# Kernel tuning notes

Hardware: AMD Instinct MI355X
Metric: run time of the kernel (lower is better)

## Reference

```python
import jax, jax.numpy as jnp
import numpy as np

B, C, N, M = 8, 128, 2048, 512

def setup_inputs() -> dict:
    key = jax.random.key(0)
    k1, k2, k3, k4 = jax.random.split(key, 4)
    scale = 1.0 / np.sqrt(C)
    x = jax.random.normal(k1, (B, C, N), dtype=jnp.float32)
    # conv1d with kernel size 1 and no bias == channel-mixing matmul, weight [C_out, C_in]
    Wq = jax.random.normal(k2, (C, C), dtype=jnp.float32) * scale
    Wk = jax.random.normal(k3, (C, C), dtype=jnp.float32) * scale
    Wv = jax.random.normal(k4, (C, C), dtype=jnp.float32) * scale
    return {"x": x, "Wq": Wq, "Wk": Wk, "Wv": Wv, "npts_ds": M}

def reference(x, Wq, Wk, Wv, npts_ds):
    # q,k,v: [B,C,N] via 1x1 conv == einsum over input channels
    q = jnp.einsum('oc,bcn->bon', Wq, x)
    k = jnp.einsum('oc,bcn->bon', Wk, x)
    v = jnp.einsum('oc,bcn->bon', Wv, x)
    # energy: [B,N,N] = q^T k (contract channel dim)
    energy = jnp.einsum('bcn,bcm->bnm', q, k)
    scale_factor = jnp.sqrt(jnp.asarray(q.shape[-2], dtype=energy.dtype))  # sqrt(C)
    attention = jax.nn.softmax(energy / scale_factor, axis=-1)  # [B,N,N]
    selection = jnp.sum(attention, axis=-2)  # [B,N] column sums
    _, idx = jax.lax.top_k(selection, npts_ds)  # [B,M]
    # gather selected attention rows: [B,M,N]
    scores = jnp.take_along_axis(attention, idx[:, :, None], axis=1)
    # weighted sum of values: [B,M,C]
    out = jnp.einsum('bmn,bcn->bcm', scores, v)  # [B,C,M]
    return out
```

## Files before the change

### kernel.cpp

```cpp
#include <hip/hip_runtime.h>
#include <math.h>

namespace {
constexpr int B = 8, C = 128, N = 2048, M = 512;
constexpr int NSPLIT = 8;
constexpr int MBLK = 16;
constexpr float INV_SQRT_C = 0.08838834764831845f;
}

typedef __attribute__((ext_vector_type(8))) short short8;
typedef __attribute__((ext_vector_type(16))) float f32x16;
typedef unsigned short ushort_t;
typedef unsigned int u32;

__device__ inline ushort_t f2bf(float f) {
  union { float f; u32 u; } a; a.f = f;
  u32 r = a.u + 0x7fffu + ((a.u >> 16) & 1u);
  return (ushort_t)(r >> 16);
}
__device__ inline float bf2f(ushort_t h) {
  union { u32 u; float f; } a; a.u = ((u32)h) << 16; return a.f;
}

__device__ __forceinline__ void gl_lds16(const ushort_t* g, ushort_t* l) {
  __builtin_amdgcn_global_load_lds(
      (const __attribute__((address_space(1))) unsigned int*)g,
      (__attribute__((address_space(3))) unsigned int*)l, 16, 0, 0);
}

__global__ __launch_bounds__(256) void qkv_kernel(
    const float* __restrict__ x, const float* __restrict__ Wq,
    const float* __restrict__ Wk, const float* __restrict__ Wv,
    ushort_t* __restrict__ split, ushort_t* __restrict__ vbf) {
  const size_t TERM = (size_t)B * N * C;
  int kc = blockIdx.x;
  int o0 = kc * 8;
  int n = blockIdx.y * 256 + threadIdx.x;
  int b = blockIdx.z;
  const float* xb = x + (size_t)b * C * N + n;
  float aq[8] = {}, ak[8] = {}, av[8] = {};
  #pragma unroll 4
  for (int c = 0; c < C; ++c) {
    float xv = xb[(size_t)c * N];
    #pragma unroll
    for (int j = 0; j < 8; ++j) {
      aq[j] = fmaf(Wq[(o0 + j) * C + c], xv, aq[j]);
      ak[j] = fmaf(Wk[(o0 + j) * C + c], xv, ak[j]);
      av[j] = fmaf(Wv[(o0 + j) * C + c], xv, av[j]);
    }
  }
  #pragma unroll
  for (int j = 0; j < 8; ++j)
    vbf[((size_t)b * C + o0 + j) * N + n] = f2bf(av[j]);
  size_t rowoff = ((size_t)b * 16 + kc) * (size_t)N * 8 + (size_t)n * 8;
  #pragma unroll
  for (int tt = 0; tt < 3; ++tt) {
    short8 qv, kv;
    #pragma unroll
    for (int j = 0; j < 8; ++j) {
      ushort_t h = f2bf(aq[j]); qv[j] = (short)h; aq[j] -= bf2f(h);
      h = f2bf(ak[j]);          kv[j] = (short)h; ak[j] -= bf2f(h);
    }
    *(short8*)&split[tt * TERM + rowoff]       = qv;
    *(short8*)&split[(3 + tt) * TERM + rowoff] = kv;
  }
}

__global__ __launch_bounds__(256) void energy_kernel(
    const ushort_t* __restrict__ split,
    float* __restrict__ Ae, float* __restrict__ rowpart) {
  __shared__ __align__(16) union {
    ushort_t stg[2][12288];
    struct { float red[128][64]; float red2[128][2]; } r;
  } sm;
  const size_t TERM = (size_t)B * N * C;
  const size_t ROW8 = (size_t)N * 8;
  int t = threadIdx.x;
  int lane = t & 63, w = t >> 6;
  int wn = w & 1, wm = w >> 1;
  int lin = blockIdx.y * 16 + blockIdx.x;
  int st = lin >> 4, wi = lin & 15;
  int mb = (st & 3) * 4 + (wi & 3);
  int nb = (st >> 2) * 4 + (wi >> 2);
  int m0 = mb * 128, n0 = nb * 128, b = blockIdx.z;
  int lr = lane & 31, lq = lane >> 5;

  const ushort_t* gA = split + (size_t)b * 16 * ROW8
                     + (size_t)(t >> 7) * ROW8 + ((size_t)n0 + (t & 127)) * 8;
  const ushort_t* gB = split + 3 * TERM + (size_t)b * 16 * ROW8
                     + (size_t)(t >> 7) * ROW8 + ((size_t)m0 + (t & 127)) * 8;

  f32x16 acc[2][2] = {};
  #pragma unroll
  for (int tt = 0; tt < 3; ++tt) {
    gl_lds16(gA + (size_t)tt * TERM, &sm.stg[0][tt * 2048 + t * 8]);
    gl_lds16(gB + (size_t)tt * TERM, &sm.stg[0][(3 + tt) * 2048 + t * 8]);
  }
  __syncthreads();

  const int aoff = (lq * 128 + wn * 64 + lr) * 8;
  const int boff = (lq * 128 + wm * 64 + lr) * 8;
  #pragma unroll
  for (int s = 0; s < 8; ++s) {
    const int cur = s & 1;
    if (s < 7) {
      size_t so = (size_t)(2 * (s + 1)) * ROW8;
      #pragma unroll
      for (int tt = 0; tt < 3; ++tt) {
        gl_lds16(gA + (size_t)tt * TERM + so, &sm.stg[cur ^ 1][tt * 2048 + t * 8]);
        gl_lds16(gB + (size_t)tt * TERM + so, &sm.stg[cur ^ 1][(3 + tt) * 2048 + t * 8]);
      }
    }
    short8 aT[3][2], bT[3][2];
    #pragma unroll
    for (int tt = 0; tt < 3; ++tt)
      #pragma unroll
      for (int i = 0; i < 2; ++i) {
        aT[tt][i] = *(const short8*)&sm.stg[cur][tt * 2048 + aoff + i * 256];
        bT[tt][i] = *(const short8*)&sm.stg[cur][(3 + tt) * 2048 + boff + i * 256];
      }
    #pragma unroll
    for (int mt = 0; mt < 2; ++mt)
      #pragma unroll
      for (int nt = 0; nt < 2; ++nt) {
        acc[mt][nt] = __builtin_amdgcn_mfma_f32_32x32x16_bf16(aT[0][mt], bT[0][nt], acc[mt][nt], 0, 0, 0);
        acc[mt][nt] = __builtin_amdgcn_mfma_f32_32x32x16_bf16(aT[1][mt], bT[0][nt], acc[mt][nt], 0, 0, 0);
        acc[mt][nt] = __builtin_amdgcn_mfma_f32_32x32x16_bf16(aT[0][mt], bT[1][nt], acc[mt][nt], 0, 0, 0);
        acc[mt][nt] = __builtin_amdgcn_mfma_f32_32x32x16_bf16(aT[2][mt], bT[0][nt], acc[mt][nt], 0, 0, 0);
        acc[mt][nt] = __builtin_amdgcn_mfma_f32_32x32x16_bf16(aT[1][mt], bT[1][nt], acc[mt][nt], 0, 0, 0);
        acc[mt][nt] = __builtin_amdgcn_mfma_f32_32x32x16_bf16(aT[0][mt], bT[2][nt], acc[mt][nt], 0, 0, 0);
      }
    __syncthreads();
  }
  int lc = lr;
  #pragma unroll
  for (int mt = 0; mt < 2; ++mt) {
    #pragma unroll
    for (int reg = 0; reg < 16; ++reg) {
      int row = (reg & 3) + 8 * (reg >> 2) + 4 * lq;
      int rloc = wn * 64 + mt * 32 + row;
      float e0 = expf(acc[mt][0][reg] * INV_SQRT_C);
      float e1 = expf(acc[mt][1][reg] * INV_SQRT_C);
      float* pA = Ae + ((size_t)b * N + n0 + rloc) * N + m0 + wm * 64 + lc;
      pA[0] = e0; pA[32] = e1;
      sm.r.red[rloc][wm * 32 + lc] = e0 + e1;
    }
  }
  __syncthreads();
  {
    int row = t >> 1, h = t & 1;
    float ssum = 0.f;
    #pragma unroll
    for (int j0 = 0; j0 < 32; ++j0) {
      int j = (j0 + (t & 31)) & 31;
      ssum += sm.r.red[row][h * 32 + j];
    }
    sm.r.red2[row][h] = ssum;
  }
  __syncthreads();
  if (t < 128)
    rowpart[(size_t)mb * (B * N) + b * N + n0 + t] = sm.r.red2[t][0] + sm.r.red2[t][1];
}

__global__ __launch_bounds__(256) void colsum_kernel(
    const float* __restrict__ Ae, const float* __restrict__ rowpart,
    float* __restrict__ selpart) {
  __shared__ float sinv[256];
  int t = threadIdx.x;
  int m = blockIdx.x * 256 + t;
  int nch = blockIdx.y, b = blockIdx.z;
  int n0 = nch * (N / 8);
  {
    int n = n0 + t;
    float s = 0.f;
    #pragma unroll
    for (int sl = 0; sl < MBLK; ++sl)
      s += rowpart[(size_t)sl * (B * N) + b * N + n];
    sinv[t] = 1.0f / s;
  }
  __syncthreads();
  const float* Ab = Ae + (size_t)b * N * N;
  float acc = 0.f;
  #pragma unroll 8
  for (int n = n0; n < n0 + N / 8; ++n)
    acc = fmaf(Ab[(size_t)n * N + m], sinv[n - n0], acc);
  selpart[(size_t)nch * (B * N) + b * N + m] = acc;
}

__global__ __launch_bounds__(256) void topk_kernel(
    const float* __restrict__ selpart, int* __restrict__ idx) {
  __shared__ float s[N];
  __shared__ int rsum[64][4];
  int b = blockIdx.y;
  int t = threadIdx.x;
  for (int i = t; i < N; i += 256) {
    float v_ = 0.f;
    #pragma unroll
    for (int nch = 0; nch < 8; ++nch)
      v_ += selpart[(size_t)nch * (B * N) + b * N + i];
    s[i] = v_;
  }
  __syncthreads();
  int i = blockIdx.x * 64 + (t & 63);
  int jc = t >> 6;
  float val = s[i];
  int r = 0;
  for (int j = jc * 512; j < jc * 512 + 512; ++j) {
    float sj = s[j];
    r += (sj > val || (sj == val && j < i)) ? 1 : 0;
  }
  rsum[t & 63][jc] = r;
  __syncthreads();
  if (t < 64) {
    int rank = rsum[t][0] + rsum[t][1] + rsum[t][2] + rsum[t][3];
    if (rank < M) idx[b * M + rank] = blockIdx.x * 64 + t;
  }
}

__global__ __launch_bounds__(256) void out_kernel(
    const float* __restrict__ Ae, const float* __restrict__ rowpart,
    const ushort_t* __restrict__ vbf, const int* __restrict__ idx,
    float* __restrict__ part) {
  __shared__ ushort_t sc[64][72];
  __shared__ ushort_t vt[128][72];
  __shared__ int ridx[64];
  __shared__ float rinv[64];
  int t = threadIdx.x;
  int m0 = blockIdx.x * 64;
  int ns = blockIdx.y;
  int b = blockIdx.z;
  if (t < 64) {
    int r = idx[b * M + m0 + t];
    ridx[t] = r;
    float s = 0.f;
    #pragma unroll
    for (int sl = 0; sl < MBLK; ++sl)
      s += rowpart[(size_t)sl * (B * N) + b * N + r];
    rinv[t] = 1.0f / s;
  }
  __syncthreads();
  int lane = t & 63, w = t >> 6;
  int wc = w & 1, wm = w >> 1;
  int lr = lane & 31, lq = lane >> 5;
  f32x16 acc[2] = {};
  int nbeg = ns * (N / NSPLIT);
  for (int kb = 0; kb < N / NSPLIT; kb += 64) {
    __syncthreads();
    #pragma unroll
    for (int it = 0; it < 16; ++it) {
      int ii = it * 256 + t;
      int r = ii >> 6, cn = ii & 63;
      float sv = Ae[((size_t)b * N + ridx[r]) * N + nbeg + kb + cn] * rinv[r];
      sc[r][cn] = f2bf(sv);
    }
    #pragma unroll
    for (int it = 0; it < 4; ++it) {
      int u = it * 256 + t;
      int r = u >> 3, seg = u & 7;
      *(short8*)&vt[r][seg * 8] =
          *(const short8*)&vbf[((size_t)b * C + r) * N + nbeg + kb + seg * 8];
    }
    __syncthreads();
    #pragma unroll
    for (int ks = 0; ks < 4; ++ks) {
      short8 bf_ = *(const short8*)&sc[wm * 32 + lr][ks * 16 + lq * 8];
      #pragma unroll
      for (int ct = 0; ct < 2; ++ct) {
        short8 af = *(const short8*)&vt[wc * 64 + ct * 32 + lr][ks * 16 + lq * 8];
        acc[ct] = __builtin_amdgcn_mfma_f32_32x32x16_bf16(af, bf_, acc[ct], 0, 0, 0);
      }
    }
  }
  float* pb = part + ((size_t)ns * B + b) * C * M;
  #pragma unroll
  for (int ct = 0; ct < 2; ++ct) {
    #pragma unroll
    for (int reg = 0; reg < 16; ++reg) {
      int crow = wc * 64 + ct * 32 + (reg & 3) + 8 * (reg >> 2) + 4 * lq;
      pb[(size_t)crow * M + m0 + wm * 32 + lr] = acc[ct][reg];
    }
  }
}

__global__ __launch_bounds__(256) void reduce_kernel(
    const float* __restrict__ part, float* __restrict__ out) {
  int i = (blockIdx.x * 256 + threadIdx.x) * 4;
  float4 a = make_float4(0.f, 0.f, 0.f, 0.f);
  #pragma unroll
  for (int ns = 0; ns < NSPLIT; ++ns) {
    float4 p = *(const float4*)&part[(size_t)ns * (B * C * M) + i];
    a.x += p.x; a.y += p.y; a.z += p.z; a.w += p.w;
  }
  *(float4*)&out[i] = a;
}

extern "C" void kernel_launch(void* const* d_in, const int* in_sizes, int n_in,
                              void* d_out, int out_size, void* d_ws, size_t ws_size,
                              hipStream_t stream) {
  const float* x  = (const float*)d_in[0];
  const float* Wq = (const float*)d_in[1];
  const float* Wk = (const float*)d_in[2];
  const float* Wv = (const float*)d_in[3];
  float* out = (float*)d_out;

  const size_t TSZ = (size_t)B * N * C;
  ushort_t* split = (ushort_t*)d_ws;
  ushort_t* vbf   = split + 6 * TSZ;
  float* Ae       = (float*)(vbf + TSZ);
  float* rowpart  = Ae + (size_t)B * N * N;
  float* selpart  = rowpart + (size_t)MBLK * B * N;
  int*   idx      = (int*)(selpart + (size_t)8 * B * N);
  float* part     = (float*)split;

  qkv_kernel<<<dim3(16, N / 256, B), 256, 0, stream>>>(x, Wq, Wk, Wv, split, vbf);
  energy_kernel<<<dim3(N / 128, N / 128, B), 256, 0, stream>>>(split, Ae, rowpart);
  colsum_kernel<<<dim3(N / 256, 8, B), 256, 0, stream>>>(Ae, rowpart, selpart);
  topk_kernel<<<dim3(N / 64, B), 256, 0, stream>>>(selpart, idx);
  out_kernel<<<dim3(M / 64, NSPLIT, B), 256, 0, stream>>>(Ae, rowpart, vbf, idx, part);
  reduce_kernel<<<dim3(B * C * M / 1024), 256, 0, stream>>>(part, out);
}
```

Before: 229.3 us.

## Deepen energy kernel prefetch, remap blocks per XCD, use nontemporal stores

```diff
diff --git a/kernel.cpp b/kernel.cpp
--- a/kernel.cpp
+++ b/kernel.cpp
@@ -79,7 +79,9 @@
   int lane = t & 63, w = t >> 6;
   int wn = w & 1, wm = w >> 1;
   int lin = blockIdx.y * 16 + blockIdx.x;
-  int st = lin >> 4, wi = lin & 15;
+  int xcd = lin & 7, slot = lin >> 3;
+  int st = xcd * 2 + (slot >> 4);
+  int wi = slot & 15;
   int mb = (st & 3) * 4 + (wi & 3);
   int nb = (st >> 2) * 4 + (wi >> 2);
   int m0 = mb * 128, n0 = nb * 128, b = blockIdx.z;
@@ -89,28 +91,28 @@
                      + (size_t)(t >> 7) * ROW8 + ((size_t)n0 + (t & 127)) * 8;
   const ushort_t* gB = split + 3 * TERM + (size_t)b * 16 * ROW8
                      + (size_t)(t >> 7) * ROW8 + ((size_t)m0 + (t & 127)) * 8;
-
-  f32x16 acc[2][2] = {};
-  #pragma unroll
-  for (int tt = 0; tt < 3; ++tt) {
-    gl_lds16(gA + (size_t)tt * TERM, &sm.stg[0][tt * 2048 + t * 8]);
-    gl_lds16(gB + (size_t)tt * TERM, &sm.stg[0][(3 + tt) * 2048 + t * 8]);
-  }
-  __syncthreads();
-
   const int aoff = (lq * 128 + wn * 64 + lr) * 8;
   const int boff = (lq * 128 + wm * 64 + lr) * 8;
+
+#define STAGE_STEP(buf_, s_) do {                                            \
+    size_t so_ = (size_t)(2 * (s_)) * ROW8;                                  \
+    _Pragma("unroll")                                                        \
+    for (int tt = 0; tt < 3; ++tt) {                                         \
+      gl_lds16(gA + (size_t)tt * TERM + so_, &sm.stg[buf_][tt * 2048 + t * 8]); \
+      gl_lds16(gB + (size_t)tt * TERM + so_, &sm.stg[buf_][(3 + tt) * 2048 + t * 8]); \
+    }                                                                        \
+  } while (0)
+
+  f32x16 acc[2][2] = {};
+  STAGE_STEP(0, 0);
+  STAGE_STEP(1, 1);
   #pragma unroll
   for (int s = 0; s < 8; ++s) {
     const int cur = s & 1;
-    if (s < 7) {
-      size_t so = (size_t)(2 * (s + 1)) * ROW8;
-      #pragma unroll
-      for (int tt = 0; tt < 3; ++tt) {
-        gl_lds16(gA + (size_t)tt * TERM + so, &sm.stg[cur ^ 1][tt * 2048 + t * 8]);
-        gl_lds16(gB + (size_t)tt * TERM + so, &sm.stg[cur ^ 1][(3 + tt) * 2048 + t * 8]);
-      }
-    }
+    if (s < 7) asm volatile("s_waitcnt vmcnt(6)" ::: "memory");
+    else       asm volatile("s_waitcnt vmcnt(0)" ::: "memory");
+    __builtin_amdgcn_sched_barrier(0);
+    __builtin_amdgcn_s_barrier();
     short8 aT[3][2], bT[3][2];
     #pragma unroll
     for (int tt = 0; tt < 3; ++tt)
@@ -130,8 +132,11 @@
         acc[mt][nt] = __builtin_amdgcn_mfma_f32_32x32x16_bf16(aT[1][mt], bT[1][nt], acc[mt][nt], 0, 0, 0);
         acc[mt][nt] = __builtin_amdgcn_mfma_f32_32x32x16_bf16(aT[0][mt], bT[2][nt], acc[mt][nt], 0, 0, 0);
       }
-    __syncthreads();
-  }
+    __builtin_amdgcn_sched_barrier(0);
+    __builtin_amdgcn_s_barrier();
+    if (s < 6) STAGE_STEP(cur, s + 2);
+  }
+#undef STAGE_STEP
   int lc = lr;
   #pragma unroll
   for (int mt = 0; mt < 2; ++mt) {
@@ -142,7 +147,8 @@
       float e0 = expf(acc[mt][0][reg] * INV_SQRT_C);
       float e1 = expf(acc[mt][1][reg] * INV_SQRT_C);
       float* pA = Ae + ((size_t)b * N + n0 + rloc) * N + m0 + wm * 64 + lc;
-      pA[0] = e0; pA[32] = e1;
+      __builtin_nontemporal_store(e0, pA);
+      __builtin_nontemporal_store(e1, pA + 32);
       sm.r.red[rloc][wm * 32 + lc] = e0 + e1;
     }
   }
```

Result: no change. 227.4 us, median of 4 (-0.8%).
